# Kernel tuning notes

Measured on AMD Instinct MI355X. Metric: run time of the kernel, lower is better.

## Reference

```python
import jax, jax.numpy as jnp
import numpy as np

N = 1048576   # nodes (1024x1024 fluid grid)
E = 8388608   # edges (avg degree 8)
IDX_NODE_X, IDX_NODE_Y = 0, 1
IDX_EDGE_X, IDX_EDGE_Y = 0, 1


def setup_inputs() -> dict:
    key = jax.random.key(0)
    ks = jax.random.split(key, 9)
    v_x = jax.random.normal(ks[0], (N, 2), jnp.float32)
    v_prev_x = jax.random.normal(ks[1], (N, 2), jnp.float32)
    p_x = jax.random.normal(ks[2], (N, 1), jnp.float32)
    p_prev_x = jax.random.normal(ks[3], (N, 1), jnp.float32)
    rho_x = jax.random.normal(ks[4], (N, 1), jnp.float32)
    rho_prev_x = jax.random.normal(ks[5], (N, 1), jnp.float32)
    edge_attr = jax.random.normal(ks[6], (E, 2), jnp.float32)
    # mimic grid finite-difference sparsity: ~half the entries of each
    # direction column are exactly zero, exercising the != 0 edge masking
    keep = jax.random.bernoulli(ks[7], 0.5, (E, 2))
    edge_attr = jnp.where(keep, edge_attr, 0.0)
    edge_index = jax.random.randint(ks[8], (2, E), 0, N, dtype=jnp.int64)
    return dict(
        v_x=v_x, v_prev_x=v_prev_x, p_x=p_x, p_prev_x=p_prev_x,
        rho_x=rho_x, rho_prev_x=rho_prev_x,
        M=jnp.float32(1.0), eta=jnp.float32(1.0), zeta=jnp.float32(1.0),
        dt=jnp.float32(0.01), edge_attr=edge_attr, edge_index=edge_index,
    )


def _spatial_derivative(x, src, dst, edge_attr, mask, idx_node, idx_edge, n):
    """Gather-compute-scatter finite difference: scatter-mean of
    (x[dst, idx_node] - x[src, idx_node]) / edge_attr[:, idx_edge]
    over the masked edge subset, aggregated at the source node."""
    diff = x[dst, idx_node] - x[src, idx_node]                  # [E]
    denom = jnp.where(mask, edge_attr[:, idx_edge], 1.0)        # avoid /0 on masked-out edges
    contrib = jnp.where(mask, diff / denom, 0.0)                # [E]
    sums = jax.ops.segment_sum(contrib, src, num_segments=n)    # [N]
    cnt = jax.ops.segment_sum(mask.astype(x.dtype), src, num_segments=n)
    return sums / jnp.maximum(cnt, 1.0)                         # [N]


def reference(v_x, v_prev_x, p_x, p_prev_x, rho_x, rho_prev_x, M, eta, zeta, dt, edge_attr, edge_index):
    n = v_x.shape[0]
    src, dst = edge_index[0], edge_index[1]
    vp = v_x * p_x                                  # [N,2] * [N,1] -> [N,2]
    mask_x = edge_attr[:, IDX_NODE_X] != 0          # edges with x-offset
    mask_y = edge_attr[:, IDX_NODE_Y] != 0          # edges with y-offset
    d_x = _spatial_derivative(vp, src, dst, edge_attr, mask_x, IDX_NODE_X, IDX_EDGE_X, n)
    d_y = _spatial_derivative(vp, src, dst, edge_attr, mask_y, IDX_NODE_Y, IDX_EDGE_Y, n)
    loss_continuity = (d_x + d_y)[:, None] + (p_x - p_prev_x) / dt   # [N,1]
    return loss_continuity
```

## Files before the change

kernel.cpp:

```cpp
#include <hip/hip_runtime.h>
#include <hip/hip_fp16.h>


#define NPB      2048
#define NPB_LOG  11
#define NBUCK_MAX 512
#define CE       4096
#define CB       1024
#define EPT      4
#define CCAP     4608
#define MAXCHUNK 2048
#define NHINT    4096
#define K_OFF    1073741824.0

typedef unsigned long long ull;


__global__ void node_pre_fast(const float2* __restrict__ v,
                              const float* __restrict__ p,
                              __half2* __restrict__ vph,
                              double2* __restrict__ side,
                              int* __restrict__ oflow, int N) {
    int i = blockIdx.x * blockDim.x + threadIdx.x;
    int stride = gridDim.x * blockDim.x;
    for (; i < N; i += stride) {
        float2 vi = v[i];
        float pi = p[i];
        vph[i] = __float22half2_rn(make_float2(vi.x * pi, vi.y * pi));
        side[i] = make_double2(0.0, 0.0);
    }
    if (blockIdx.x == 0 && threadIdx.x == 0) *oflow = 0;
}

__device__ __forceinline__ void route_rec(uint2 r, int k, size_t rb, int slot,
                                          uint2* __restrict__ recs,
                                          const float2* __restrict__ v,
                                          const float* __restrict__ p,
                                          double2* __restrict__ side,
                                          int* __restrict__ oflow) {
    if (slot < CCAP) { recs[rb + slot] = r; return; }
    unsigned sl = r.x & (NPB - 1u);
    bool diry = (r.x >> 11) & 1u;
    int d = (int)(r.x >> 12);
    float a = __uint_as_float(r.y);
    int s = k * NPB + (int)sl;
    float2 vd = v[d], vs = v[s];
    float pd = p[d], ps = p[s];
    float c = (diry ? vd.y * pd - vs.y * ps : vd.x * pd - vs.x * ps) / a;
    unsafeAtomicAdd(diry ? &side[s].y : &side[s].x, (double)c + K_OFF);
    atomicOr(oflow, 1);
}

__global__ __launch_bounds__(CB) void chunk_sort(
        const float2* __restrict__ ea,
        const int* __restrict__ src_idx,
        const int* __restrict__ dst_idx,
        const float2* __restrict__ v,
        const float* __restrict__ p,
        uint2* __restrict__ recs,
        unsigned short* __restrict__ off_mat,
        unsigned short* __restrict__ cnt_mat,
        double2* __restrict__ side,
        int* __restrict__ oflow,
        int nbuck, int E) {
    __shared__ uint2 stage[CCAP];
    __shared__ int hist[NBUCK_MAX];
    __shared__ int tl[NBUCK_MAX];
    __shared__ int cur[NBUCK_MAX];
    int c = blockIdx.x, t = threadIdx.x;
    int e0 = c * CE;

    uint2 R0[EPT], R1[EPT];
    int K[EPT], NR[EPT];
#pragma unroll
    for (int i = 0; i < EPT; ++i) {
        int e = e0 + i * CB + t;
        NR[i] = 0; K[i] = 0;
        if (e < E) {
            float2 a = ea[e];
            bool mx = (a.x != 0.f);
            bool my = (a.y != 0.f);
            if (mx || my) {
                int s = src_idx[e];
                int d = dst_idx[e];
                K[i] = s >> NPB_LOG;
                unsigned sl = (unsigned)(s & (NPB - 1));
                unsigned dm = (unsigned)d << 12;
                NR[i] = (int)mx + (int)my;
                uint2 rx = make_uint2(sl | dm, __float_as_uint(a.x));
                uint2 ry = make_uint2(sl | 0x800u | dm, __float_as_uint(a.y));
                R0[i] = mx ? rx : ry;
                R1[i] = ry;
            }
        }
    }
    if (t < nbuck) hist[t] = 0;
    __syncthreads();
#pragma unroll
    for (int i = 0; i < EPT; ++i)
        if (NR[i]) atomicAdd(&hist[K[i]], NR[i]);
    __syncthreads();
    if (t < nbuck) tl[t] = hist[t];
    __syncthreads();
    for (int off = 1; off < NBUCK_MAX; off <<= 1) {
        int x = 0;
        if (t < nbuck && t >= off) x = tl[t - off];
        __syncthreads();
        if (t < nbuck) tl[t] += x;
        __syncthreads();
    }
    int total = tl[nbuck - 1];
    if (t < nbuck) {
        int excl = tl[t] - hist[t];
        cur[t] = excl;
        off_mat[(size_t)c * nbuck + t] = (unsigned short)excl;
        cnt_mat[(size_t)c * nbuck + t] = (unsigned short)hist[t];
    }
    __syncthreads();
    size_t rb = (size_t)c * CCAP;
    if (total <= CCAP) {
#pragma unroll
        for (int i = 0; i < EPT; ++i)
            if (NR[i]) {
                int slot = atomicAdd(&cur[K[i]], NR[i]);
                stage[slot] = R0[i];
                if (NR[i] == 2) stage[slot + 1] = R1[i];
            }
        __syncthreads();
        for (int j = t; j < total; j += CB) recs[rb + j] = stage[j];
    } else {
#pragma unroll
        for (int i = 0; i < EPT; ++i)
            if (NR[i]) {
                int slot = atomicAdd(&cur[K[i]], NR[i]);
                route_rec(R0[i], K[i], rb, slot, recs, v, p, side, oflow);
                if (NR[i] == 2) route_rec(R1[i], K[i], rb, slot + 1, recs, v, p, side, oflow);
            }
    }
}

__global__ __launch_bounds__(1024) void bucket_reduce(
        const uint2* __restrict__ recs,
        const unsigned short* __restrict__ off_mat,
        const unsigned short* __restrict__ cnt_mat,
        const float2* __restrict__ v,
        const float* __restrict__ p,
        const __half2* __restrict__ vph,
        const double2* __restrict__ side,
        const int* __restrict__ oflow,
        const float* __restrict__ p_prev,
        const float* __restrict__ dt_ptr,
        float* __restrict__ out,
        int nchunk, int nbuck, int N) {
    __shared__ float2 vps[NPB];
    __shared__ double2 acc[NPB];
    __shared__ int glen[MAXCHUNK];
    __shared__ int goff[MAXCHUNK];
    __shared__ unsigned short hint[NHINT];
    __shared__ int s_of;
    int k = blockIdx.x, t = threadIdx.x;
    int g0 = k * NPB;
    for (int i = t; i < NPB; i += 1024) {
        int g = g0 + i;
        float2 vi = (g < N) ? v[g] : make_float2(0.f, 0.f);
        float pi = (g < N) ? p[g] : 0.f;
        vps[i] = make_float2(vi.x * pi, vi.y * pi);
        acc[i] = make_double2(0.0, 0.0);
    }
    if (t == 0) s_of = *oflow;
    for (int c = t; c < MAXCHUNK; c += 1024) {
        int len = 0, off = 0;
        if (c < nchunk) {
            off = __builtin_nontemporal_load(&off_mat[(size_t)c * nbuck + k]);
            int cnt = __builtin_nontemporal_load(&cnt_mat[(size_t)c * nbuck + k]);
            len = min(cnt, max(0, CCAP - off));
        }
        goff[c] = off;
        glen[c] = len;
    }
    __syncthreads();
    for (int off = 1; off < MAXCHUNK; off <<= 1) {
        int i0 = t, i1 = t + 1024;
        int x0 = (i0 >= off) ? glen[i0 - off] : 0;
        int x1 = glen[i1 - off];
        __syncthreads();
        glen[i0] += x0;
        glen[i1] += x1;
        __syncthreads();
    }
    int total = glen[MAXCHUNK - 1];
    int nh = min((total + 7) >> 3, NHINT);
    for (int j = t; j < nh; j += 1024) {
        int target = j << 3;
        int lo = 0, hi = nchunk - 1;
        while (lo < hi) {
            int mid = (lo + hi) >> 1;
            if (glen[mid] > target) hi = mid; else lo = mid + 1;
        }
        hint[j] = (unsigned short)lo;
    }
    __syncthreads();
    const ull* recs64 = (const ull*)recs;
    for (int idx = t; idx < total; idx += 1024) {
        int j = idx >> 3;
        int cur;
        if (j < NHINT) {
            cur = hint[j];
        } else {
            int lo = 0, hi = nchunk - 1;
            while (lo < hi) {
                int mid = (lo + hi) >> 1;
                if (glen[mid] > idx) hi = mid; else lo = mid + 1;
            }
            cur = lo;
        }
        while (glen[cur] <= idx) ++cur;
        int pre = cur ? glen[cur - 1] : 0;
        ull rv = __builtin_nontemporal_load(
            &recs64[(size_t)cur * CCAP + goff[cur] + (idx - pre)]);
        unsigned m = (unsigned)rv;
        float a = __uint_as_float((unsigned)(rv >> 32));
        int sl = (int)(m & (NPB - 1u));
        bool diry = (m >> 11) & 1u;
        int d = (int)(m >> 12);
        float2 vpd = __half22float2(vph[d]);
        float2 vs = vps[sl];
        float c = (diry ? vpd.y - vs.y : vpd.x - vs.x) / a;
        unsafeAtomicAdd(diry ? &acc[sl].y : &acc[sl].x, (double)c + K_OFF);
    }
    __syncthreads();
    float inv_dt = 1.0f / dt_ptr[0];
    for (int i = t; i < NPB; i += 1024) {
        int g = g0 + i;
        if (g < N) {
            double2 A = acc[i];
            if (s_of) {
                double2 S = side[g];
                A.x += S.x; A.y += S.y;
            }
            double cx = rint(A.x * (1.0 / K_OFF));
            double sx = A.x - cx * K_OFF;
            double cy = rint(A.y * (1.0 / K_OFF));
            double sy = A.y - cy * K_OFF;
            out[g] = (float)(sx / fmax(cx, 1.0)) + (float)(sy / fmax(cy, 1.0))
                   + (p[g] - p_prev[g]) * inv_dt;
        }
    }
}


__global__ void fb_node_pre(const float2* __restrict__ v,
                            const float* __restrict__ p,
                            float2* __restrict__ vp,
                            double2* __restrict__ acc, int N) {
    int i = blockIdx.x * blockDim.x + threadIdx.x;
    int stride = gridDim.x * blockDim.x;
    for (; i < N; i += stride) {
        float2 vi = v[i];
        float pi = p[i];
        vp[i] = make_float2(vi.x * pi, vi.y * pi);
        acc[i] = make_double2(0.0, 0.0);
    }
}

__global__ void fb_edge_scatter(const float2* __restrict__ vp,
                                const float2* __restrict__ ea,
                                const int* __restrict__ src_idx,
                                const int* __restrict__ dst_idx,
                                double2* __restrict__ acc, int E) {
    int e = blockIdx.x * blockDim.x + threadIdx.x;
    if (e >= E) return;
    float2 a = ea[e];
    bool mx = (a.x != 0.f);
    bool my = (a.y != 0.f);
    if (!mx && !my) return;
    int s = src_idx[e];
    int d = dst_idx[e];
    float2 vs = vp[s];
    float2 vd = vp[d];
    double* basep = (double*)&acc[s];
    if (mx) unsafeAtomicAdd(basep + 0, (double)((vd.x - vs.x) / a.x) + K_OFF);
    if (my) unsafeAtomicAdd(basep + 1, (double)((vd.y - vs.y) / a.y) + K_OFF);
}

__global__ void fb_node_final(const double2* __restrict__ acc,
                              const float* __restrict__ p,
                              const float* __restrict__ p_prev,
                              const float* __restrict__ dt_ptr,
                              float* __restrict__ out, int N) {
    int i = blockIdx.x * blockDim.x + threadIdx.x;
    int stride = gridDim.x * blockDim.x;
    float inv_dt = 1.0f / dt_ptr[0];
    for (; i < N; i += stride) {
        double2 A = acc[i];
        double cx = rint(A.x * (1.0 / K_OFF));
        double sx = A.x - cx * K_OFF;
        double cy = rint(A.y * (1.0 / K_OFF));
        double sy = A.y - cy * K_OFF;
        out[i] = (float)(sx / fmax(cx, 1.0)) + (float)(sy / fmax(cy, 1.0))
               + (p[i] - p_prev[i]) * inv_dt;
    }
}


extern "C" void kernel_launch(void* const* d_in, const int* in_sizes, int n_in,
                              void* d_out, int out_size, void* d_ws, size_t ws_size,
                              hipStream_t stream) {
    const float2* v_x    = (const float2*)d_in[0];
    const float*  p_x    = (const float*)d_in[2];
    const float*  p_prev = (const float*)d_in[3];
    const float*  dt     = (const float*)d_in[9];
    const float2* ea     = (const float2*)d_in[10];
    const int*    eidx   = (const int*)d_in[11];

    const int N = in_sizes[2];
    const int E = in_sizes[10] / 2;
    const int* src_idx = eidx;
    const int* dst_idx = eidx + E;

    const int nbuck  = (N + NPB - 1) >> NPB_LOG;
    const int nchunk = (E + CE - 1) / CE;

    char* w = (char*)d_ws;
    __half2* vph     = (__half2*)w;   w += (size_t)N * sizeof(__half2);
    double2* side    = (double2*)w;   w += (size_t)N * sizeof(double2);
    int*     oflow   = (int*)w;       w += 16;
    unsigned short* off_mat = (unsigned short*)w;  w += (size_t)nchunk * nbuck * sizeof(unsigned short);
    unsigned short* cnt_mat = (unsigned short*)w;  w += (size_t)nchunk * nbuck * sizeof(unsigned short);
    w = (char*)(((uintptr_t)w + 15) & ~(uintptr_t)15);
    uint2*   recs    = (uint2*)w;     w += (size_t)nchunk * CCAP * sizeof(uint2);
    size_t need_fast = (size_t)(w - (char*)d_ws);

    if (nbuck <= NBUCK_MAX && nchunk <= MAXCHUNK && N <= (1 << 20)
        && ws_size >= need_fast) {
        node_pre_fast<<<2048, 256, 0, stream>>>(v_x, p_x, vph, side, oflow, N);
        chunk_sort<<<nchunk, CB, 0, stream>>>(ea, src_idx, dst_idx, v_x, p_x,
                                              recs, off_mat, cnt_mat, side,
                                              oflow, nbuck, E);
        bucket_reduce<<<nbuck, 1024, 0, stream>>>(recs, off_mat, cnt_mat,
                                                  v_x, p_x, vph, side, oflow,
                                                  p_prev, dt,
                                                  (float*)d_out, nchunk, nbuck, N);
    } else {
        float2*  fvp  = (float2*)d_ws;
        double2* facc = (double2*)((char*)d_ws + (size_t)N * sizeof(float2));
        fb_node_pre<<<2048, 256, 0, stream>>>(v_x, p_x, fvp, facc, N);
        fb_edge_scatter<<<(E + 255) / 256, 256, 0, stream>>>(
            fvp, ea, src_idx, dst_idx, facc, E);
        fb_node_final<<<2048, 256, 0, stream>>>(
            facc, p_x, p_prev, dt, (float*)d_out, N);
    }
}
```

Measured before the change: 153.7 us.

## Replace per-node side accumulator with compact spill list for overflow records

Drops the N-sized double2 side buffer, which node_pre_fast had to zero on every call. Overflow records from chunk_sort now go to a compact global spill list, and each bucket_reduce block scans that list for its own bucket. It also adds nontemporal loads for v, p and p_prev and removes the binary-search fallback for hint lookup. The main cost removed is the 16 MB zeroing write and the conditional side read. In exchange, every block scans the whole spill list, and dropping the fallback assumes the hint table covers all records.

Measured after the change: 157.2 us. 2.2% more time.

```diff
diff --git a/kernel.cpp b/kernel.cpp
--- a/kernel.cpp
+++ b/kernel.cpp
@@ -11,57 +11,45 @@
 #define CCAP     4608
 #define MAXCHUNK 2048
 #define NHINT    4096
+#define SPILLCAP (1 << 20)
 #define K_OFF    1073741824.0
 
 typedef unsigned long long ull;
+typedef float vfloat2 __attribute__((ext_vector_type(2)));
 
 
 __global__ void node_pre_fast(const float2* __restrict__ v,
                               const float* __restrict__ p,
                               __half2* __restrict__ vph,
-                              double2* __restrict__ side,
-                              int* __restrict__ oflow, int N) {
+                              int* __restrict__ spill_cnt, int N) {
     int i = blockIdx.x * blockDim.x + threadIdx.x;
     int stride = gridDim.x * blockDim.x;
     for (; i < N; i += stride) {
         float2 vi = v[i];
         float pi = p[i];
         vph[i] = __float22half2_rn(make_float2(vi.x * pi, vi.y * pi));
-        side[i] = make_double2(0.0, 0.0);
-    }
-    if (blockIdx.x == 0 && threadIdx.x == 0) *oflow = 0;
+    }
+    if (blockIdx.x == 0 && threadIdx.x == 0) *spill_cnt = 0;
 }
 
 __device__ __forceinline__ void route_rec(uint2 r, int k, size_t rb, int slot,
                                           uint2* __restrict__ recs,
-                                          const float2* __restrict__ v,
-                                          const float* __restrict__ p,
-                                          double2* __restrict__ side,
-                                          int* __restrict__ oflow) {
+                                          uint4* __restrict__ spill,
+                                          int* __restrict__ spill_cnt) {
     if (slot < CCAP) { recs[rb + slot] = r; return; }
-    unsigned sl = r.x & (NPB - 1u);
-    bool diry = (r.x >> 11) & 1u;
-    int d = (int)(r.x >> 12);
-    float a = __uint_as_float(r.y);
-    int s = k * NPB + (int)sl;
-    float2 vd = v[d], vs = v[s];
-    float pd = p[d], ps = p[s];
-    float c = (diry ? vd.y * pd - vs.y * ps : vd.x * pd - vs.x * ps) / a;
-    unsafeAtomicAdd(diry ? &side[s].y : &side[s].x, (double)c + K_OFF);
-    atomicOr(oflow, 1);
+    int sp = atomicAdd(spill_cnt, 1);
+    if (sp < SPILLCAP) spill[sp] = make_uint4(r.x, r.y, (unsigned)k, 0u);
 }
 
 __global__ __launch_bounds__(CB) void chunk_sort(
         const float2* __restrict__ ea,
         const int* __restrict__ src_idx,
         const int* __restrict__ dst_idx,
-        const float2* __restrict__ v,
-        const float* __restrict__ p,
         uint2* __restrict__ recs,
         unsigned short* __restrict__ off_mat,
         unsigned short* __restrict__ cnt_mat,
-        double2* __restrict__ side,
-        int* __restrict__ oflow,
+        uint4* __restrict__ spill,
+        int* __restrict__ spill_cnt,
         int nbuck, int E) {
     __shared__ uint2 stage[CCAP];
     __shared__ int hist[NBUCK_MAX];
@@ -133,8 +121,8 @@
         for (int i = 0; i < EPT; ++i)
             if (NR[i]) {
                 int slot = atomicAdd(&cur[K[i]], NR[i]);
-                route_rec(R0[i], K[i], rb, slot, recs, v, p, side, oflow);
-                if (NR[i] == 2) route_rec(R1[i], K[i], rb, slot + 1, recs, v, p, side, oflow);
+                route_rec(R0[i], K[i], rb, slot, recs, spill, spill_cnt);
+                if (NR[i] == 2) route_rec(R1[i], K[i], rb, slot + 1, recs, spill, spill_cnt);
             }
     }
 }
@@ -146,8 +134,8 @@
         const float2* __restrict__ v,
         const float* __restrict__ p,
         const __half2* __restrict__ vph,
-        const double2* __restrict__ side,
-        const int* __restrict__ oflow,
+        const uint4* __restrict__ spill,
+        const int* __restrict__ spill_cnt,
         const float* __restrict__ p_prev,
         const float* __restrict__ dt_ptr,
         float* __restrict__ out,
@@ -157,17 +145,18 @@
     __shared__ int glen[MAXCHUNK];
     __shared__ int goff[MAXCHUNK];
     __shared__ unsigned short hint[NHINT];
-    __shared__ int s_of;
+    __shared__ int s_sp;
     int k = blockIdx.x, t = threadIdx.x;
     int g0 = k * NPB;
+    const vfloat2* vv = (const vfloat2*)v;
     for (int i = t; i < NPB; i += 1024) {
         int g = g0 + i;
-        float2 vi = (g < N) ? v[g] : make_float2(0.f, 0.f);
-        float pi = (g < N) ? p[g] : 0.f;
+        vfloat2 vi = (g < N) ? __builtin_nontemporal_load(&vv[g]) : (vfloat2)(0.f);
+        float pi = (g < N) ? __builtin_nontemporal_load(&p[g]) : 0.f;
         vps[i] = make_float2(vi.x * pi, vi.y * pi);
         acc[i] = make_double2(0.0, 0.0);
     }
-    if (t == 0) s_of = *oflow;
+    if (t == 0) s_sp = *spill_cnt;
     for (int c = t; c < MAXCHUNK; c += 1024) {
         int len = 0, off = 0;
         if (c < nchunk) {
@@ -202,18 +191,7 @@
     __syncthreads();
     const ull* recs64 = (const ull*)recs;
     for (int idx = t; idx < total; idx += 1024) {
-        int j = idx >> 3;
-        int cur;
-        if (j < NHINT) {
-            cur = hint[j];
-        } else {
-            int lo = 0, hi = nchunk - 1;
-            while (lo < hi) {
-                int mid = (lo + hi) >> 1;
-                if (glen[mid] > idx) hi = mid; else lo = mid + 1;
-            }
-            cur = lo;
-        }
+        int cur = hint[idx >> 3];
         while (glen[cur] <= idx) ++cur;
         int pre = cur ? glen[cur - 1] : 0;
         ull rv = __builtin_nontemporal_load(
@@ -229,21 +207,34 @@
         unsafeAtomicAdd(diry ? &acc[sl].y : &acc[sl].x, (double)c + K_OFF);
     }
     __syncthreads();
+    int nsp = min(s_sp, SPILLCAP);
+    for (int i = t; i < nsp; i += 1024) {
+        uint4 r = spill[i];
+        if ((int)r.z != k) continue;
+        unsigned m = r.x;
+        float a = __uint_as_float(r.y);
+        int sl = (int)(m & (NPB - 1u));
+        bool diry = (m >> 11) & 1u;
+        int d = (int)(m >> 12);
+        float2 vpd = __half22float2(vph[d]);
+        float2 vs = vps[sl];
+        float c = (diry ? vpd.y - vs.y : vpd.x - vs.x) / a;
+        unsafeAtomicAdd(diry ? &acc[sl].y : &acc[sl].x, (double)c + K_OFF);
+    }
+    if (nsp) __syncthreads();
     float inv_dt = 1.0f / dt_ptr[0];
     for (int i = t; i < NPB; i += 1024) {
         int g = g0 + i;
         if (g < N) {
             double2 A = acc[i];
-            if (s_of) {
-                double2 S = side[g];
-                A.x += S.x; A.y += S.y;
-            }
             double cx = rint(A.x * (1.0 / K_OFF));
             double sx = A.x - cx * K_OFF;
             double cy = rint(A.y * (1.0 / K_OFF));
             double sy = A.y - cy * K_OFF;
+            float pd = __builtin_nontemporal_load(&p[g]);
+            float pp = __builtin_nontemporal_load(&p_prev[g]);
             out[g] = (float)(sx / fmax(cx, 1.0)) + (float)(sy / fmax(cy, 1.0))
-                   + (p[g] - p_prev[g]) * inv_dt;
+                   + (pd - pp) * inv_dt;
         }
     }
 }
@@ -322,23 +313,24 @@
     const int nchunk = (E + CE - 1) / CE;
 
     char* w = (char*)d_ws;
-    __half2* vph     = (__half2*)w;   w += (size_t)N * sizeof(__half2);
-    double2* side    = (double2*)w;   w += (size_t)N * sizeof(double2);
-    int*     oflow   = (int*)w;       w += 16;
+    __half2* vph      = (__half2*)w;  w += (size_t)N * sizeof(__half2);
+    int*     spill_cnt= (int*)w;      w += 16;
     unsigned short* off_mat = (unsigned short*)w;  w += (size_t)nchunk * nbuck * sizeof(unsigned short);
     unsigned short* cnt_mat = (unsigned short*)w;  w += (size_t)nchunk * nbuck * sizeof(unsigned short);
     w = (char*)(((uintptr_t)w + 15) & ~(uintptr_t)15);
-    uint2*   recs    = (uint2*)w;     w += (size_t)nchunk * CCAP * sizeof(uint2);
+    uint4*   spill    = (uint4*)w;    w += (size_t)SPILLCAP * sizeof(uint4);
+    uint2*   recs     = (uint2*)w;    w += (size_t)nchunk * CCAP * sizeof(uint2);
     size_t need_fast = (size_t)(w - (char*)d_ws);
 
     if (nbuck <= NBUCK_MAX && nchunk <= MAXCHUNK && N <= (1 << 20)
         && ws_size >= need_fast) {
-        node_pre_fast<<<2048, 256, 0, stream>>>(v_x, p_x, vph, side, oflow, N);
-        chunk_sort<<<nchunk, CB, 0, stream>>>(ea, src_idx, dst_idx, v_x, p_x,
-                                              recs, off_mat, cnt_mat, side,
-                                              oflow, nbuck, E);
+        node_pre_fast<<<2048, 256, 0, stream>>>(v_x, p_x, vph, spill_cnt, N);
+        chunk_sort<<<nchunk, CB, 0, stream>>>(ea, src_idx, dst_idx,
+                                              recs, off_mat, cnt_mat,
+                                              spill, spill_cnt, nbuck, E);
         bucket_reduce<<<nbuck, 1024, 0, stream>>>(recs, off_mat, cnt_mat,
-                                                  v_x, p_x, vph, side, oflow,
+                                                  v_x, p_x, vph,
+                                                  spill, spill_cnt,
                                                   p_prev, dt,
                                                   (float*)d_out, nchunk, nbuck, N);
     } else {
```
